# Performance work log

Hardware: AMD Instinct MI355X
Metric: run time of the kernel (lower is better)

The kernel has to match this reference:

```python
import jax, jax.numpy as jnp
import numpy as np

B, T, D, I, C, H = 8192, 128, 7, 128, 10, 64
L = 2 ** D
SUBSET = int(I * 0.8)  # feature_subset_size = 102


def setup_inputs() -> dict:
    key = jax.random.key(0)
    ks = jax.random.split(key, 7)
    x = jax.random.normal(ks[0], (B, I), dtype=jnp.float32)
    # exact feature-subset mask: SUBSET ones per (tree, depth) row
    r = jax.random.uniform(ks[1], (T, D, I))
    ranks = jnp.argsort(jnp.argsort(r, axis=-1), axis=-1)
    feature_mask = (ranks < SUBSET).astype(jnp.float32)
    thresholds = jax.random.normal(ks[2], (T, D), dtype=jnp.float32)
    leaf_outputs = jax.random.normal(ks[3], (T, L, C), dtype=jnp.float32)
    W1 = jax.random.normal(ks[4], (I, H), dtype=jnp.float32) * 0.08
    b1 = jnp.zeros((H,), dtype=jnp.float32)
    W2 = jax.random.normal(ks[5], (H, T), dtype=jnp.float32) * 0.12
    b2 = jnp.zeros((T,), dtype=jnp.float32)
    return {"x": x, "feature_mask": feature_mask, "thresholds": thresholds,
            "leaf_outputs": leaf_outputs, "W1": W1, "b1": b1, "W2": W2, "b2": b2}


def reference(x, feature_mask, thresholds, leaf_outputs, W1, b1, W2, b2):
    depth = thresholds.shape[1]
    # split logits: masked feature sum minus threshold, per (batch, tree, depth)
    z = jnp.einsum('bi,tdi->btd', x, feature_mask) - thresholds[None, :, :]
    s = 0.5 * (z / (1.0 + jnp.abs(z)) + 1.0)  # scaled softsign split in (0,1)
    # probabilistic path routing: doubling concat, identical to torch loop
    p = jnp.ones((x.shape[0], feature_mask.shape[0], 1), dtype=x.dtype)
    for d in range(depth):
        sd = s[:, :, d:d + 1]            # [B, T, 1]
        p = jnp.concatenate([p * sd, p * (1.0 - sd)], axis=-1)  # [B, T, 2^(d+1)]
    leaf_probs = jax.nn.softmax(leaf_outputs, axis=-1)           # [T, L, C]
    tree_outputs = jnp.einsum('btl,tlc->btc', p, leaf_probs)     # [B, T, C]
    # instance-wise attention over trees (eval mode: no dropout)
    attn = jax.nn.softmax(jax.nn.relu(x @ W1 + b1) @ W2 + b2, axis=-1)  # [B, T]
    return jnp.sum(tree_outputs * attn[:, :, None], axis=1)     # [B, C]
```

## Files before the change

kernel.cpp:

```cpp
#include <hip/hip_runtime.h>
#include <hip/hip_bf16.h>
#include <hip/hip_fp16.h>


#define BB 8192
#define TT 128
#define II 128
#define CC 10
#define HH 64

#define OFF_STH 0
#define OFF_AT  3670016
#define OFF_SP  4194304
#define OFF_LPB 8388608
#define OFF_PT  8650752

typedef __attribute__((ext_vector_type(8))) short short8;
typedef __attribute__((ext_vector_type(16))) float floatx16;

static __device__ inline unsigned int pkbf(float lo, float hi) {
  __hip_bfloat162 h = __float22bfloat162_rn(make_float2(lo, hi));
  unsigned int u;
  __builtin_memcpy(&u, &h, 4);
  return u;
}

static __device__ inline unsigned int pkh(float lo, float hi) {
  __half2 h = __float22half2_rn(make_float2(lo, hi));
  unsigned int u;
  __builtin_memcpy(&u, &h, 4);
  return u;
}

static __device__ inline short8 cvt8(float4 a, float4 b) {
  union { short8 v; unsigned int u[4]; } r;
  r.u[0] = pkbf(a.x, a.y);
  r.u[1] = pkbf(a.z, a.w);
  r.u[2] = pkbf(b.x, b.y);
  r.u[3] = pkbf(b.z, b.w);
  return r.v;
}

__global__ __launch_bounds__(256, 2) void phase1_kernel(
    const float* __restrict__ x, const float* __restrict__ mask,
    const float* __restrict__ thr, const float* __restrict__ lo,
    const float* __restrict__ W1, const float* __restrict__ b1,
    const float* __restrict__ W2, const float* __restrict__ b2,
    __half* __restrict__ sTh, __half* __restrict__ attnB,
    unsigned int* __restrict__ lpb) {
  __shared__ float smem[8704];
  const int blk = blockIdx.x;
  const int tid = threadIdx.x;
  const int wv = tid >> 6, lane = tid & 63;
  const int half = lane >> 5, l31 = lane & 31;

  if (blk < 64) {
    const int b0 = blk * 128 + wv * 32;

    short8 axf[8];
    const float* xrow = x + (size_t)(b0 + l31) * II + half * 8;
#pragma unroll
    for (int s = 0; s < 8; ++s)
      axf[s] = cvt8(*(const float4*)(xrow + s * 16),
                    *(const float4*)(xrow + s * 16 + 4));

    floatx16 acch[2];
#pragma unroll
    for (int i = 0; i < 16; ++i) { acch[0][i] = 0.f; acch[1][i] = 0.f; }
#pragma unroll
    for (int s = 0; s < 8; ++s) {
#pragma unroll
      for (int tile = 0; tile < 2; ++tile) {
        union { short8 v; unsigned int u[4]; } wf;
#pragma unroll
        for (int jp = 0; jp < 4; ++jp) {
          int k0 = s * 16 + half * 8 + jp * 2;
          float f0 = W1[(size_t)k0 * HH + tile * 32 + l31];
          float f1 = W1[(size_t)(k0 + 1) * HH + tile * 32 + l31];
          wf.u[jp] = pkbf(f0, f1);
        }
        acch[tile] = __builtin_amdgcn_mfma_f32_32x32x16_bf16(
            axf[s], wf.v, acch[tile], 0, 0, 0);
      }
    }
    float* hids = smem + wv * 2176;
#pragma unroll
    for (int tile = 0; tile < 2; ++tile) {
      float bh = b1[tile * 32 + l31];
#pragma unroll
      for (int r = 0; r < 16; ++r) {
        int row = (r & 3) + 8 * (r >> 2) + 4 * half;
        hids[row * 68 + tile * 32 + l31] = fmaxf(acch[tile][r] + bh, 0.f);
      }
    }
    __syncthreads();

    short8 ahf[4];
#pragma unroll
    for (int s = 0; s < 4; ++s) {
      const float* hr = hids + l31 * 68 + s * 16 + half * 8;
      ahf[s] = cvt8(*(const float4*)hr, *(const float4*)(hr + 4));
    }

    floatx16 accl[4];
#pragma unroll
    for (int tile = 0; tile < 4; ++tile) {
#pragma unroll
      for (int i = 0; i < 16; ++i) accl[tile][i] = 0.f;
#pragma unroll
      for (int s = 0; s < 4; ++s) {
        union { short8 v; unsigned int u[4]; } wf;
#pragma unroll
        for (int jp = 0; jp < 4; ++jp) {
          int k0 = s * 16 + half * 8 + jp * 2;
          float f0 = W2[(size_t)k0 * TT + tile * 32 + l31];
          float f1 = W2[(size_t)(k0 + 1) * TT + tile * 32 + l31];
          wf.u[jp] = pkbf(f0, f1);
        }
        accl[tile] = __builtin_amdgcn_mfma_f32_32x32x16_bf16(
            ahf[s], wf.v, accl[tile], 0, 0, 0);
      }
      float bt = b2[tile * 32 + l31];
#pragma unroll
      for (int i = 0; i < 16; ++i) accl[tile][i] += bt;
    }

    float mrow[16];
#pragma unroll
    for (int r = 0; r < 16; ++r)
      mrow[r] = fmaxf(fmaxf(accl[0][r], accl[1][r]),
                      fmaxf(accl[2][r], accl[3][r]));
#pragma unroll
    for (int msk = 1; msk <= 16; msk <<= 1)
#pragma unroll
      for (int r = 0; r < 16; ++r)
        mrow[r] = fmaxf(mrow[r], __shfl_xor(mrow[r], msk, 64));
    float srow[16];
#pragma unroll
    for (int r = 0; r < 16; ++r) srow[r] = 0.f;
#pragma unroll
    for (int tile = 0; tile < 4; ++tile)
#pragma unroll
      for (int r = 0; r < 16; ++r) {
        float e = __expf(accl[tile][r] - mrow[r]);
        accl[tile][r] = e;
        srow[r] += e;
      }
#pragma unroll
    for (int msk = 1; msk <= 16; msk <<= 1)
#pragma unroll
      for (int r = 0; r < 16; ++r)
        srow[r] += __shfl_xor(srow[r], msk, 64);
#pragma unroll
    for (int r = 0; r < 16; ++r) srow[r] = 1.f / srow[r];

#pragma unroll
    for (int tile = 0; tile < 4; ++tile)
#pragma unroll
      for (int r = 0; r < 16; ++r) {
        int row = (r & 3) + 8 * (r >> 2) + 4 * half;
        attnB[(size_t)(b0 + row) * TT + tile * 32 + l31] =
            __float2half(accl[tile][r] * srow[r]);
      }

  } else if (blk < 960) {
    const int blk2 = blk - 64;
    const int mb = blk2 >> 5;
    const int ns = blk2 & 31;
    const int m0 = mb * 32;

    short8 af[8];
    const float* mrow = mask + (size_t)(m0 + l31) * II + half * 8;
#pragma unroll
    for (int s = 0; s < 8; ++s)
      af[s] = cvt8(*(const float4*)(mrow + s * 16),
                   *(const float4*)(mrow + s * 16 + 4));
    float th[16];
#pragma unroll
    for (int r = 0; r < 16; ++r)
      th[r] = thr[m0 + (r & 3) + 8 * (r >> 2) + 4 * half];

#pragma unroll
    for (int nb = 0; nb < 2; ++nb) {
      const int n0 = ns * 256 + wv * 64 + nb * 32;
      const float* xrow = x + (size_t)(n0 + l31) * II + half * 8;
      floatx16 acc;
#pragma unroll
      for (int i = 0; i < 16; ++i) acc[i] = 0.f;
#pragma unroll
      for (int s = 0; s < 8; ++s) {
        short8 bf = cvt8(*(const float4*)(xrow + s * 16),
                         *(const float4*)(xrow + s * 16 + 4));
        acc = __builtin_amdgcn_mfma_f32_32x32x16_bf16(af[s], bf, acc, 0, 0, 0);
      }
#pragma unroll
      for (int r = 0; r < 16; ++r) {
        int row = (r & 3) + 8 * (r >> 2) + 4 * half;
        float z = acc[r] - th[r];
        float o = 0.5f * (z / (1.f + fabsf(z)) + 1.f);
        sTh[(size_t)(m0 + row) * BB + n0 + l31] = __float2half(o);
      }
    }

  } else {
    float* lps = smem;
    const int t0 = (blk - 960) * 2;
    {
      int tl = tid >> 7, l = tid & 127;
      const float* row = lo + ((size_t)(t0 + tl) * 128 + l) * CC;
      float v[CC];
      float m = -1e30f;
#pragma unroll
      for (int c = 0; c < CC; ++c) { v[c] = row[c]; m = fmaxf(m, v[c]); }
      float s = 0.f;
#pragma unroll
      for (int c = 0; c < CC; ++c) { v[c] = __expf(v[c] - m); s += v[c]; }
      float inv = 1.f / s;
      float* o = lps + (tl * 128 + l) * 12;
#pragma unroll
      for (int c = 0; c < CC; ++c) o[c] = v[c] * inv;
      o[10] = 0.f; o[11] = 0.f;
    }
    __syncthreads();

#pragma unroll
    for (int jj = 0; jj < 4; ++jj) {
      int idx = tid + 256 * jj;
      int tl = idx >> 9, rem = idx & 511;
      int s = rem >> 6, ln = rem & 63;
      int hf = ln >> 5, n = ln & 31;
      unsigned int wd[4];
#pragma unroll
      for (int jp = 0; jp < 4; ++jp) {
        int l0 = s * 16 + hf * 8 + jp * 2;
        float f0 = (n < CC) ? lps[(tl * 128 + l0) * 12 + n] : 0.f;
        float f1 = (n < CC) ? lps[(tl * 128 + l0 + 1) * 12 + n] : 0.f;
        wd[jp] = pkh(f0, f1);
      }
      ((uint4*)lpb)[(size_t)(t0 + tl) * 512 + s * 64 + ln] =
          make_uint4(wd[0], wd[1], wd[2], wd[3]);
    }
  }
}

__global__ __launch_bounds__(256) void repack_kernel(
    const __half* __restrict__ sTh, __half* __restrict__ sPack) {
  int idx = blockIdx.x * 256 + threadIdx.x;
  int b = idx & (BB - 1);
  int t = idx >> 13;
  union { uint4 v; __half h[8]; } p;
#pragma unroll
  for (int d = 0; d < 7; ++d)
    p.h[d] = sTh[(size_t)(t * 7 + d) * BB + b];
  p.h[7] = __float2half(0.f);
  ((uint4*)sPack)[(size_t)t * BB + b] = p.v;
}

__global__ __launch_bounds__(256, 4) void main_kernel(
    const __half* __restrict__ sPack, const __half* __restrict__ attnB,
    const unsigned int* __restrict__ lpb, float* __restrict__ partial) {
  __shared__ float red[128 * 10];
  const int bg = blockIdx.x, tg = blockIdx.y;
  const int tid = threadIdx.x;
  const int w = tid >> 6, lane = tid & 63;
  const int half = lane >> 5;
  const int b = bg * 128 + w * 32 + (lane & 31);
  const uint4* spk = (const uint4*)sPack;

  __half av[8];
  *(uint4*)av = *(const uint4*)(attnB + (size_t)b * TT + tg * 8);

  floatx16 acc;
#pragma unroll
  for (int i = 0; i < 16; ++i) acc[i] = 0.f;

  uint4 sv[2];
  sv[0] = spk[(size_t)(tg * 8) * BB + b];

#pragma unroll
  for (int it = 0; it < 8; ++it) {
    const int cur = it & 1;
    const int t = tg * 8 + it;
    uint4 bf[8];
    const uint4* lpt = (const uint4*)lpb + (size_t)t * 512 + lane;
#pragma unroll
    for (int s = 0; s < 8; ++s) bf[s] = lpt[s * 64];
    if (it < 7) sv[cur ^ 1] = spk[(size_t)(t + 1) * BB + b];

    const __half* sh = (const __half*)&sv[cur];
    float s0 = __half2float(sh[0]), s1 = __half2float(sh[1]);
    float s2 = __half2float(sh[2]), s3 = __half2float(sh[3]);
    float s4 = __half2float(sh[4]), s5 = __half2float(sh[5]);
    float s6 = __half2float(sh[6]);
    float A  = __half2float(av[it]);

    float s0c = 1.f - s0, s1c = 1.f - s1, s2c = 1.f - s2;
    float t0 = s0 * s1, t1 = s0c * s1, t2 = s0 * s1c, t3 = s0c * s1c;
    float pl[8];
    pl[0] = t0 * s2;  pl[1] = t1 * s2;  pl[2] = t2 * s2;  pl[3] = t3 * s2;
    pl[4] = t0 * s2c; pl[5] = t1 * s2c; pl[6] = t2 * s2c; pl[7] = t3 * s2c;
    float sel3 = half ? (1.f - s3) : s3;
    float Af = A * sel3;
    float s4c = 1.f - s4, s5c = 1.f - s5;
    float as6 = Af * s6, as6c = Af * (1.f - s6);
    float u0 = s4 * s5, u1 = s4c * s5, u2 = s4 * s5c, u3 = s4c * s5c;
    float wv[8];
    wv[0] = u0 * as6;  wv[1] = u1 * as6;  wv[2] = u2 * as6;  wv[3] = u3 * as6;
    wv[4] = u0 * as6c; wv[5] = u1 * as6c; wv[6] = u2 * as6c; wv[7] = u3 * as6c;

    __half2 pl2[4];
#pragma unroll
    for (int jp = 0; jp < 4; ++jp)
      pl2[jp] = __float22half2_rn(make_float2(pl[jp * 2], pl[jp * 2 + 1]));

#pragma unroll
    for (int s = 0; s < 8; ++s) {
      __half2 w2 = __half2half2(__float2half(wv[s]));
      union { short8 v; __half2 h[4]; } a;
#pragma unroll
      for (int jp = 0; jp < 4; ++jp) a.h[jp] = __hmul2(pl2[jp], w2);
      acc = __builtin_amdgcn_mfma_f32_32x32x16_f16(
          a.v, *(const short8*)&bf[s], acc, 0, 0, 0);
    }
  }

  const int col = lane & 31;
  if (col < CC) {
#pragma unroll
    for (int r = 0; r < 16; ++r) {
      int row = (r & 3) + 8 * (r >> 2) + 4 * half;
      red[(w * 32 + row) * 10 + col] = acc[r];
    }
  }
  __syncthreads();
#pragma unroll
  for (int j = 0; j < 5; ++j) {
    int idx = tid + 256 * j;
    partial[(size_t)tg * 81920 + (size_t)bg * 1280 + idx] = red[idx];
  }
}

__global__ __launch_bounds__(256) void reduce_kernel(
    const float* __restrict__ partial, float* __restrict__ out) {
  int idx = blockIdx.x * 256 + threadIdx.x;
  float s = 0.f;
#pragma unroll
  for (int tg = 0; tg < 16; ++tg) s += partial[(size_t)tg * 81920 + idx];
  out[idx] = s;
}

extern "C" void kernel_launch(void* const* d_in, const int* in_sizes, int n_in,
                              void* d_out, int out_size, void* d_ws, size_t ws_size,
                              hipStream_t stream) {
  const float* x    = (const float*)d_in[0];
  const float* mask = (const float*)d_in[1];
  const float* thr  = (const float*)d_in[2];
  const float* lo   = (const float*)d_in[3];
  const float* W1   = (const float*)d_in[4];
  const float* b1   = (const float*)d_in[5];
  const float* W2   = (const float*)d_in[6];
  const float* b2   = (const float*)d_in[7];
  float* out = (float*)d_out;
  float* ws  = (float*)d_ws;

  __half*       sTh     = (__half*)(ws + OFF_STH);
  __half*       attnB   = (__half*)(ws + OFF_AT);
  __half*       sPack   = (__half*)(ws + OFF_SP);
  unsigned int* LPb     = (unsigned int*)(ws + OFF_LPB);
  float*        partial = ws + OFF_PT;

  phase1_kernel<<<1024, 256, 0, stream>>>(x, mask, thr, lo, W1, b1, W2, b2,
                                          sTh, attnB, LPb);
  repack_kernel<<<4096, 256, 0, stream>>>(sTh, sPack);
  main_kernel<<<dim3(64, 16), 256, 0, stream>>>(sPack, attnB, LPb, partial);
  reduce_kernel<<<320, 256, 0, stream>>>(partial, out);
}
```

Baseline: 118.3 us.

## Fuse split-logit GEMM with repack via LDS, dropping separate repack kernel

The split-probability GEMM is moved into its own kernel that tiles 28 rows (4 trees × 7 depths) per block. It packs results through shared memory straight into the [tree, batch, 8] half layout. This removes the intermediate sTh buffer, its global write and strided reread, and one kernel launch. The cost is that 4 of the 32 MFMA rows are wasted per block, and the attention/leaf-prep work now runs as a separate launch.

```diff
diff --git a/kernel.cpp b/kernel.cpp
--- a/kernel.cpp
+++ b/kernel.cpp
@@ -9,11 +9,10 @@
 #define CC 10
 #define HH 64
 
-#define OFF_STH 0
-#define OFF_AT  3670016
-#define OFF_SP  4194304
-#define OFF_LPB 8388608
-#define OFF_PT  8650752
+#define OFF_SP  0
+#define OFF_AT  4194304
+#define OFF_LPB 4718592
+#define OFF_PT  4980736
 
 typedef __attribute__((ext_vector_type(8))) short short8;
 typedef __attribute__((ext_vector_type(16))) float floatx16;
@@ -41,13 +40,72 @@
   return r.v;
 }
 
-__global__ __launch_bounds__(256, 2) void phase1_kernel(
-    const float* __restrict__ x, const float* __restrict__ mask,
-    const float* __restrict__ thr, const float* __restrict__ lo,
+__global__ __launch_bounds__(256, 4) void zs_kernel(
+    const float* __restrict__ mask, const float* __restrict__ x,
+    const float* __restrict__ thr, __half* __restrict__ sPack) {
+  __shared__ __half lds[4 * 256 * 8];
+  const int ns = blockIdx.x;
+  const int mb = blockIdx.y;
+  const int tid = threadIdx.x;
+  const int wv = tid >> 6, lane = tid & 63;
+  const int half = lane >> 5, l31 = lane & 31;
+  const int m0 = mb * 28;
+
+  int mr = m0 + l31; if (mr > 895) mr = 895;
+  const float* mrow = mask + (size_t)mr * II + half * 8;
+  short8 af[8];
+#pragma unroll
+  for (int s = 0; s < 8; ++s)
+    af[s] = cvt8(*(const float4*)(mrow + s * 16),
+                 *(const float4*)(mrow + s * 16 + 4));
+  float th[16];
+#pragma unroll
+  for (int r = 0; r < 16; ++r) {
+    int m = m0 + (r & 3) + 8 * (r >> 2) + 4 * half;
+    th[r] = thr[m > 895 ? 895 : m];
+  }
+
+#pragma unroll
+  for (int nb = 0; nb < 2; ++nb) {
+    const int nl = wv * 64 + nb * 32;
+    const float* xrow = x + (size_t)(ns * 256 + nl + l31) * II + half * 8;
+    floatx16 acc;
+#pragma unroll
+    for (int i = 0; i < 16; ++i) acc[i] = 0.f;
+#pragma unroll
+    for (int s = 0; s < 8; ++s) {
+      short8 bf = cvt8(*(const float4*)(xrow + s * 16),
+                       *(const float4*)(xrow + s * 16 + 4));
+      acc = __builtin_amdgcn_mfma_f32_32x32x16_bf16(af[s], bf, acc, 0, 0, 0);
+    }
+#pragma unroll
+    for (int r = 0; r < 16; ++r) {
+      int row = (r & 3) + 8 * (r >> 2) + 4 * half;
+      if (row < 28) {
+        int tl = row / 7;
+        int d = row - tl * 7;
+        float z = acc[r] - th[r];
+        float o = 0.5f * (z / (1.f + fabsf(z)) + 1.f);
+        lds[(tl * 256 + nl + l31) * 8 + d] = __float2half(o);
+      }
+    }
+  }
+  __syncthreads();
+
+  const uint4* l4 = (const uint4*)lds;
+#pragma unroll
+  for (int j = 0; j < 4; ++j) {
+    int idx = tid + 256 * j;
+    ((uint4*)sPack)[(size_t)(4 * mb + (idx >> 8)) * BB + ns * 256 + (idx & 255)] =
+        l4[idx];
+  }
+}
+
+__global__ __launch_bounds__(256, 2) void attn_prep_kernel(
+    const float* __restrict__ x, const float* __restrict__ lo,
     const float* __restrict__ W1, const float* __restrict__ b1,
     const float* __restrict__ W2, const float* __restrict__ b2,
-    __half* __restrict__ sTh, __half* __restrict__ attnB,
-    unsigned int* __restrict__ lpb) {
+    __half* __restrict__ attnB, unsigned int* __restrict__ lpb) {
   __shared__ float smem[8704];
   const int blk = blockIdx.x;
   const int tid = threadIdx.x;
@@ -163,48 +221,9 @@
             __float2half(accl[tile][r] * srow[r]);
       }
 
-  } else if (blk < 960) {
-    const int blk2 = blk - 64;
-    const int mb = blk2 >> 5;
-    const int ns = blk2 & 31;
-    const int m0 = mb * 32;
-
-    short8 af[8];
-    const float* mrow = mask + (size_t)(m0 + l31) * II + half * 8;
-#pragma unroll
-    for (int s = 0; s < 8; ++s)
-      af[s] = cvt8(*(const float4*)(mrow + s * 16),
-                   *(const float4*)(mrow + s * 16 + 4));
-    float th[16];
-#pragma unroll
-    for (int r = 0; r < 16; ++r)
-      th[r] = thr[m0 + (r & 3) + 8 * (r >> 2) + 4 * half];
-
-#pragma unroll
-    for (int nb = 0; nb < 2; ++nb) {
-      const int n0 = ns * 256 + wv * 64 + nb * 32;
-      const float* xrow = x + (size_t)(n0 + l31) * II + half * 8;
-      floatx16 acc;
-#pragma unroll
-      for (int i = 0; i < 16; ++i) acc[i] = 0.f;
-#pragma unroll
-      for (int s = 0; s < 8; ++s) {
-        short8 bf = cvt8(*(const float4*)(xrow + s * 16),
-                         *(const float4*)(xrow + s * 16 + 4));
-        acc = __builtin_amdgcn_mfma_f32_32x32x16_bf16(af[s], bf, acc, 0, 0, 0);
-      }
-#pragma unroll
-      for (int r = 0; r < 16; ++r) {
-        int row = (r & 3) + 8 * (r >> 2) + 4 * half;
-        float z = acc[r] - th[r];
-        float o = 0.5f * (z / (1.f + fabsf(z)) + 1.f);
-        sTh[(size_t)(m0 + row) * BB + n0 + l31] = __float2half(o);
-      }
-    }
-
   } else {
     float* lps = smem;
-    const int t0 = (blk - 960) * 2;
+    const int t0 = (blk - 64) * 2;
     {
       int tl = tid >> 7, l = tid & 127;
       const float* row = lo + ((size_t)(t0 + tl) * 128 + l) * CC;
@@ -241,19 +260,6 @@
           make_uint4(wd[0], wd[1], wd[2], wd[3]);
     }
   }
-}
-
-__global__ __launch_bounds__(256) void repack_kernel(
-    const __half* __restrict__ sTh, __half* __restrict__ sPack) {
-  int idx = blockIdx.x * 256 + threadIdx.x;
-  int b = idx & (BB - 1);
-  int t = idx >> 13;
-  union { uint4 v; __half h[8]; } p;
-#pragma unroll
-  for (int d = 0; d < 7; ++d)
-    p.h[d] = sTh[(size_t)(t * 7 + d) * BB + b];
-  p.h[7] = __float2half(0.f);
-  ((uint4*)sPack)[(size_t)t * BB + b] = p.v;
 }
 
 __global__ __launch_bounds__(256, 4) void main_kernel(
@@ -363,15 +369,13 @@
   float* out = (float*)d_out;
   float* ws  = (float*)d_ws;
 
-  __half*       sTh     = (__half*)(ws + OFF_STH);
+  __half*       sPack   = (__half*)(ws + OFF_SP);
   __half*       attnB   = (__half*)(ws + OFF_AT);
-  __half*       sPack   = (__half*)(ws + OFF_SP);
   unsigned int* LPb     = (unsigned int*)(ws + OFF_LPB);
   float*        partial = ws + OFF_PT;
 
-  phase1_kernel<<<1024, 256, 0, stream>>>(x, mask, thr, lo, W1, b1, W2, b2,
-                                          sTh, attnB, LPb);
-  repack_kernel<<<4096, 256, 0, stream>>>(sTh, sPack);
+  zs_kernel<<<dim3(32, 32), 256, 0, stream>>>(mask, x, thr, sPack);
+  attn_prep_kernel<<<128, 256, 0, stream>>>(x, lo, W1, b1, W2, b2, attnB, LPb);
   main_kernel<<<dim3(64, 16), 256, 0, stream>>>(sPack, attnB, LPb, partial);
   reduce_kernel<<<320, 256, 0, stream>>>(partial, out);
 }
```

After: 124.5 us. +5.3%, slower.
